# Performance work log

Measured on AMD Instinct MI355X. Metric: run time of the kernel, lower is better.

The kernel has to match this reference:

```python
import jax, jax.numpy as jnp
import numpy as np

N_NODES = 20000
N_EDGES = 160000
N_GRAPHS = 100
IN_CH = 64
EDGE_DIM = 8
NEG_SLOPE = 0.2


def _gatv2(x, edge_index, edge_attr, Wl, Wr, We, att, b, heads, ch, n_nodes):
    # GATv2Conv: e_ij = att . leaky_relu(Wl x_j + Wr x_i [+ We e_ij]), softmax over dst i,
    # out_i = sum_j alpha_ij * (Wl x_j), concat heads, + bias.
    src, dst = edge_index[0], edge_index[1]
    xl = (x @ Wl).reshape(-1, heads, ch)  # [N,H,C] source-side transform
    xr = (x @ Wr).reshape(-1, heads, ch)  # [N,H,C] target-side transform
    m = xl[src] + xr[dst]                 # [E,H,C]
    if edge_attr is not None:
        m = m + (edge_attr @ We).reshape(-1, heads, ch)
    m = jax.nn.leaky_relu(m, NEG_SLOPE)
    logit = jnp.einsum('ehc,hc->eh', m, att)                     # [E,H]
    mx = jax.ops.segment_max(logit, dst, num_segments=n_nodes)   # [N,H]
    ex = jnp.exp(logit - mx[dst])
    den = jax.ops.segment_sum(ex, dst, num_segments=n_nodes)     # [N,H]
    alpha = ex / (den[dst] + 1e-16)                              # [E,H]
    out = jax.ops.segment_sum(alpha[:, :, None] * xl[src], dst, num_segments=n_nodes)
    return out.reshape(-1, heads * ch) + b


def setup_inputs() -> dict:
    key = jax.random.key(0)
    ks = jax.random.split(key, 24)
    def rn(k, shape, fan_in):
        return jax.random.normal(k, shape, dtype=jnp.float32) / np.sqrt(fan_in)
    inp = {}
    inp['x'] = jax.random.normal(ks[0], (N_NODES, IN_CH), dtype=jnp.float32)
    inp['edge_attr'] = jax.random.uniform(ks[1], (N_EDGES, EDGE_DIM), dtype=jnp.float32)
    inp['Wl1'] = rn(ks[2], (IN_CH, 1024), IN_CH)
    inp['Wr1'] = rn(ks[3], (IN_CH, 1024), IN_CH)
    inp['We1'] = rn(ks[4], (EDGE_DIM, 1024), EDGE_DIM)
    inp['att1'] = rn(ks[5], (4, 256), 256)
    inp['b1'] = jnp.zeros((1024,), jnp.float32)
    inp['Wl2'] = rn(ks[6], (1024, 256), 1024)
    inp['Wr2'] = rn(ks[7], (1024, 256), 1024)
    inp['We2'] = rn(ks[8], (EDGE_DIM, 256), EDGE_DIM)
    inp['att2'] = rn(ks[9], (4, 64), 64)
    inp['b2'] = jnp.zeros((256,), jnp.float32)
    inp['Wlp'] = rn(ks[10], (256, 384), 256)
    inp['Wrp'] = rn(ks[11], (256, 384), 256)
    inp['attp'] = rn(ks[12], (6, 64), 64)
    inp['bp'] = jnp.zeros((384,), jnp.float32)
    inp['Wfc1'] = rn(ks[13], (384, 64), 384)
    inp['bfc1'] = jnp.zeros((64,), jnp.float32)
    inp['Wfc2'] = rn(ks[14], (64, 1), 64)
    inp['bfc2'] = jnp.zeros((1,), jnp.float32)
    inp['edge_index'] = jax.random.randint(ks[15], (2, N_EDGES), 0, N_NODES, dtype=jnp.int32)
    inp['edge_index_master'] = jax.random.randint(ks[16], (2, N_EDGES), 0, N_NODES, dtype=jnp.int32)
    inp['n_nodes'] = jnp.full((N_GRAPHS,), N_NODES // N_GRAPHS, dtype=jnp.int32)
    return inp


def reference(x, edge_attr, Wl1, Wr1, We1, att1, b1, Wl2, Wr2, We2, att2, b2,
              Wlp, Wrp, attp, bp, Wfc1, bfc1, Wfc2, bfc2,
              edge_index, edge_index_master, n_nodes):
    h = _gatv2(x, edge_index, edge_attr, Wl1, Wr1, We1, att1, b1, 4, 256, N_NODES)
    h = jax.nn.relu(h)
    h = _gatv2(h, edge_index, edge_attr, Wl2, Wr2, We2, att2, b2, 4, 64, N_NODES)
    h = jax.nn.relu(h)
    h = _gatv2(h, edge_index_master, None, Wlp, Wrp, None, attp, bp, 6, 64, N_NODES)
    last_idx = jnp.cumsum(n_nodes) - 1          # master node = last node of each graph
    master = h[last_idx]                        # [G,384] (dropout p=0 -> identity)
    z = jax.nn.relu(master @ Wfc1 + bfc1)
    return z @ Wfc2 + bfc2                      # [G,1]
```

## Files before the change

### kernel.cpp

```cpp
#include <hip/hip_runtime.h>
#include <hip/hip_bf16.h>

#define DIV_UP(a,b) (((a)+(b)-1)/(b))

typedef __attribute__((ext_vector_type(8))) short short8;
typedef __attribute__((ext_vector_type(4))) float floatx4;
typedef _Float16 half2t __attribute__((ext_vector_type(2)));

static __device__ __forceinline__ unsigned short f2bf(float v) {
    unsigned u = __builtin_bit_cast(unsigned, v);
    u += 0x7fffu + ((u >> 16) & 1u);
    return (unsigned short)(u >> 16);
}
static __device__ __forceinline__ float bflo(unsigned v) {
    return __builtin_bit_cast(float, v << 16);
}
static __device__ __forceinline__ float bfhi(unsigned v) {
    return __builtin_bit_cast(float, v & 0xffff0000u);
}
static __device__ __forceinline__ float fexp2(float x) { return __builtin_amdgcn_exp2f(x); }

static __device__ __forceinline__ unsigned packh2(float lo, float hi) {
    half2t h; h[0] = (_Float16)lo; h[1] = (_Float16)hi;
    return __builtin_bit_cast(unsigned, h);
}
static __device__ __forceinline__ float fdot2(unsigned a, unsigned b, float c) {
    return __builtin_amdgcn_fdot2(__builtin_bit_cast(half2t, a),
                                  __builtin_bit_cast(half2t, b), c, false);
}
static __device__ __forceinline__ unsigned uget(const uint4 v, int k) {
    return k == 0 ? v.x : k == 1 ? v.y : k == 2 ? v.z : v.w;
}

template <int CPL> struct RawT;
template <> struct RawT<8> { using T = uint4; };
template <> struct RawT<4> { using T = uint2; };
template <> struct RawT<2> { using T = unsigned; };

template <int CPL>
static __device__ __forceinline__ void unpackx(const typename RawT<CPL>::T& v, float* d) {
    if constexpr (CPL == 8) {
        d[0] = bflo(v.x); d[1] = bfhi(v.x);
        d[2] = bflo(v.y); d[3] = bfhi(v.y);
        d[4] = bflo(v.z); d[5] = bfhi(v.z);
        d[6] = bflo(v.w); d[7] = bfhi(v.w);
    } else if constexpr (CPL == 4) {
        d[0] = bflo(v.x); d[1] = bfhi(v.x);
        d[2] = bflo(v.y); d[3] = bfhi(v.y);
    } else {
        d[0] = bflo(v); d[1] = bfhi(v);
    }
}

template <int CPL>
static __device__ __forceinline__ void store_bf16v(unsigned short* p, const float* s) {
    unsigned short tmp[CPL];
#pragma unroll
    for (int c = 0; c < CPL; ++c) tmp[c] = f2bf(s[c]);
    if constexpr (CPL == 8) *(uint4*)p = *(uint4*)tmp;
    else if constexpr (CPL == 4) *(ushort4*)p = *(ushort4*)tmp;
    else if constexpr (CPL == 2) *(ushort2*)p = *(ushort2*)tmp;
    else p[0] = tmp[0];
}

template <int CTRL>
static __device__ __forceinline__ float dpp_mv(float x) {
    int r = __builtin_amdgcn_update_dpp(0, __builtin_bit_cast(int, x), CTRL, 0xF, 0xF, false);
    return __builtin_bit_cast(float, r);
}
template <int G>
static __device__ __forceinline__ float group_reduce(float x) {
    x += dpp_mv<0xB1>(x);
    x += dpp_mv<0x4E>(x);
    x += dpp_mv<0x124>(x);
    x += dpp_mv<0x128>(x);
    if constexpr (G >= 32) x += __shfl_xor(x, 16, 64);
    if constexpr (G >= 64) x += __shfl_xor(x, 32, 64);
    return x;
}

static __device__ __forceinline__ void tr_pair(const float* Wa, const float* Wb, int K, int Nn,
                                               unsigned short* Wt, int i) {
    int tot = K * Nn;
    const float* W = (i < tot) ? Wa : Wb;
    unsigned short* dst = Wt + ((i < tot) ? 0 : (size_t)Nn * K);
    int ii = (i < tot) ? i : i - tot;
    int k = ii % K, n = ii / K;
    dst[(size_t)n * K + k] = f2bf(W[(size_t)k * Nn + n]);
}

__global__ void prep_all(const float* __restrict__ x,
                         const float* __restrict__ Wl1, const float* __restrict__ Wr1,
                         const float* __restrict__ Wl2, const float* __restrict__ Wr2,
                         const float* __restrict__ Wlp, const float* __restrict__ Wrp,
                         unsigned short* __restrict__ xbf,
                         unsigned short* __restrict__ wt1, unsigned short* __restrict__ wt2,
                         unsigned short* __restrict__ wt3, int N) {
    const int S1 = 2 * 64 * 1024, S2 = 2 * 1024 * 256, S3 = 2 * 256 * 384;
    int id = blockIdx.x * blockDim.x + threadIdx.x;
    if (id < S1) tr_pair(Wl1, Wr1, 64, 1024, wt1, id);
    else if (id < S1 + S2) tr_pair(Wl2, Wr2, 1024, 256, wt2, id - S1);
    else if (id < S1 + S2 + S3) tr_pair(Wlp, Wrp, 256, 384, wt3, id - S1 - S2);
    else {
        int i = id - S1 - S2 - S3;
        if (i < N * 64) xbf[i] = f2bf(x[i]);
    }
}

#define GLOAD_LDS16(gp, lp) \
    __builtin_amdgcn_global_load_lds((const __attribute__((address_space(1))) void*)(gp), \
                                     (__attribute__((address_space(3))) void*)(lp), 16, 0, 0)

__global__ __launch_bounds__(256) void gemm_mfma(
    const unsigned short* __restrict__ A, const unsigned short* __restrict__ Bt,
    unsigned short* __restrict__ CL, unsigned short* __restrict__ CR,
    int M, int NL, int K) {
    __shared__ unsigned short As[128 * 32];
    __shared__ unsigned short Bs[128 * 32];
    const int tid = threadIdx.x;
    const int m0 = blockIdx.y * 128, n0 = blockIdx.x * 128;
    const bool left = (n0 < NL);
    unsigned short* Cb = left ? CL : CR;
    const int nbase = left ? n0 : n0 - NL;
    const int wave = tid >> 6, lane = tid & 63;
    const int wm = (wave >> 1) * 64, wn = (wave & 1) * 64;
    const int r15 = lane & 15, quad = lane >> 4;
    const int srow = lane >> 2, scol = (lane & 3) * 8;
    const int arow0 = m0 + 32 * wave + srow;
    const int brow0 = n0 + 32 * wave + srow;
    const unsigned short* ap0 = A + (size_t)arow0 * K + scol;
    const unsigned short* ap1 = ap0 + (size_t)16 * K;
    const unsigned short* bp0 = Bt + (size_t)brow0 * K + scol;
    const unsigned short* bp1 = bp0 + (size_t)16 * K;
    unsigned short* alds0 = As + (32 * wave) * 32;
    unsigned short* alds1 = alds0 + 16 * 32;
    unsigned short* blds0 = Bs + (32 * wave) * 32;
    unsigned short* blds1 = blds0 + 16 * 32;
    const bool av0 = arow0 < M, av1 = (arow0 + 16) < M;
    floatx4 acc[4][4];
#pragma unroll
    for (int i = 0; i < 4; ++i)
#pragma unroll
        for (int j = 0; j < 4; ++j) acc[i][j] = (floatx4)0.f;

    for (int k0 = 0; k0 < K; k0 += 32) {
        if (av0) GLOAD_LDS16(ap0, alds0);
        if (av1) GLOAD_LDS16(ap1, alds1);
        GLOAD_LDS16(bp0, blds0);
        GLOAD_LDS16(bp1, blds1);
        ap0 += 32; ap1 += 32; bp0 += 32; bp1 += 32;
        __syncthreads();
        short8 af[4], bfr[4];
#pragma unroll
        for (int i = 0; i < 4; ++i)
            af[i] = *(const short8*)(&As[(wm + i * 16 + r15) * 32 + quad * 8]);
#pragma unroll
        for (int j = 0; j < 4; ++j)
            bfr[j] = *(const short8*)(&Bs[(wn + j * 16 + r15) * 32 + quad * 8]);
#pragma unroll
        for (int i = 0; i < 4; ++i)
#pragma unroll
            for (int j = 0; j < 4; ++j)
                acc[i][j] = __builtin_amdgcn_mfma_f32_16x16x32_bf16(af[i], bfr[j], acc[i][j], 0, 0, 0);
        __syncthreads();
    }
#pragma unroll
    for (int i = 0; i < 4; ++i)
#pragma unroll
        for (int j = 0; j < 4; ++j)
#pragma unroll
            for (int r = 0; r < 4; ++r) {
                int m = m0 + wm + i * 16 + quad * 4 + r;
                int n = nbase + wn + j * 16 + r15;
                if (m < M) Cb[(size_t)m * NL + n] = f2bf(acc[i][j][r]);
            }
}

__global__ void count2_kernel(const int* __restrict__ dst0, const int* __restrict__ dst1,
                              int E, int N, int* __restrict__ cnt) {
    int e = blockIdx.x * blockDim.x + threadIdx.x;
    if (e < E) atomicAdd(&cnt[dst0[e]], 1);
    else if (e < 2 * E) atomicAdd(&cnt[N + dst1[e - E]], 1);
}

__global__ __launch_bounds__(1024) void scan_kernel(const int* __restrict__ cnt_all, int N,
                                                    int* __restrict__ off_all, int* __restrict__ cur_all) {
    const int* cnt = cnt_all + blockIdx.x * N;
    int* off = off_all + blockIdx.x * (N + 1);
    int* cur = cur_all + blockIdx.x * N;
    __shared__ int part[1024];
    int t = threadIdx.x;
    int per = (N + 1023) >> 10;
    int base = t * per;
    int s = 0;
    for (int i = 0; i < per; ++i) { int idx = base + i; if (idx < N) s += cnt[idx]; }
    part[t] = s;
    __syncthreads();
    for (int d2 = 1; d2 < 1024; d2 <<= 1) {
        int v = (t >= d2) ? part[t - d2] : 0;
        __syncthreads();
        part[t] += v;
        __syncthreads();
    }
    int pre = (t == 0) ? 0 : part[t - 1];
    for (int i = 0; i < per; ++i) {
        int idx = base + i;
        if (idx < N) { off[idx] = pre; cur[idx] = pre; pre += cnt[idx]; }
    }
    if (t == 1023) off[N] = part[1023];
}

__global__ void fill2_kernel(const int* __restrict__ src0, const int* __restrict__ dst0,
                             const int* __restrict__ src1, const int* __restrict__ dst1,
                             int E, int N, int* __restrict__ cur, int2* __restrict__ edges,
                             int* __restrict__ srcs) {
    int e = blockIdx.x * blockDim.x + threadIdx.x;
    if (e < E) {
        int p = atomicAdd(&cur[dst0[e]], 1);
        edges[p] = make_int2(src0[e], e);
        srcs[p] = src0[e];
    } else if (e < 2 * E) {
        int i = e - E;
        int p = atomicAdd(&cur[N + dst1[i]], 1);
        srcs[E + p] = src1[i];
    }
}

__global__ void ea_gather_kernel(const float* __restrict__ ea, const int2* __restrict__ edges,
                                 uint4* __restrict__ ead, int E) {
    int j = blockIdx.x * blockDim.x + threadIdx.x;
    if (j >= E) return;
    int ey = edges[j].y;
    const float4* s = (const float4*)(ea + (size_t)ey * 8);
    float4 a = s[0], b = s[1];
    uint4 o;
    o.x = packh2(a.x, a.y);
    o.y = packh2(a.z, a.w);
    o.z = packh2(b.x, b.y);
    o.w = packh2(b.z, b.w);
    ead[j] = o;
}

template <int D, int CPL, int G, int NE>
static __device__ __forceinline__ void hase_group(
    const unsigned short* __restrict__ xl, const uint4* __restrict__ ej,
    const int* __restrict__ sj, const unsigned* wbu,
    const float (&att_r)[CPL], const float (&xr_r)[CPL], int c0,
    float& m, float& l, float (&acc)[CPL]) {
    int src[NE];
#pragma unroll
    for (int n = 0; n < NE; ++n) src[n] = sj[n];
    uint4 ev[NE];
#pragma unroll
    for (int n = 0; n < NE; ++n) ev[n] = ej[n];
    float xv[NE][CPL], z[NE][CPL];
#pragma unroll
    for (int n = 0; n < NE; ++n) {
        typename RawT<CPL>::T xw =
            *(const typename RawT<CPL>::T*)(xl + (size_t)src[n] * D + c0);
        unpackx<CPL>(xw, xv[n]);
#pragma unroll
        for (int c = 0; c < CPL; ++c) z[n][c] = xv[n][c] + xr_r[c];
    }
#pragma unroll
    for (int kp = 0; kp < 4; ++kp) {
#pragma unroll
        for (int q = 0; q < CPL / 4; ++q) {
            uint4 w4 = *(const uint4*)(wbu + kp * D + q * 256);
#pragma unroll
            for (int n = 0; n < NE; ++n) {
                unsigned ep = uget(ev[n], kp);
                z[n][q * 4 + 0] = fdot2(ep, w4.x, z[n][q * 4 + 0]);
                z[n][q * 4 + 1] = fdot2(ep, w4.y, z[n][q * 4 + 1]);
                z[n][q * 4 + 2] = fdot2(ep, w4.z, z[n][q * 4 + 2]);
                z[n][q * 4 + 3] = fdot2(ep, w4.w, z[n][q * 4 + 3]);
            }
        }
    }
    float lg[NE];
#pragma unroll
    for (int n = 0; n < NE; ++n) {
        float t = 0.f;
#pragma unroll
        for (int c = 0; c < CPL; ++c) {
            float a = z[n][c] > 0.f ? z[n][c] : 0.2f * z[n][c];
            t = fmaf(att_r[c], a, t);
        }
        lg[n] = group_reduce<G>(t);
    }
    float mn = m;
#pragma unroll
    for (int n = 0; n < NE; ++n) mn = fmaxf(mn, lg[n]);
    float sc = fexp2(m - mn);
    float p[NE], ps = 0.f;
#pragma unroll
    for (int n = 0; n < NE; ++n) { p[n] = fexp2(lg[n] - mn); ps += p[n]; }
    m = mn;
    l = fmaf(l, sc, ps);
#pragma unroll
    for (int c = 0; c < CPL; ++c) {
        float t = p[0] * xv[0][c];
#pragma unroll
        for (int n = 1; n < NE; ++n) t = fmaf(p[n], xv[n][c], t);
        acc[c] = fmaf(acc[c], sc, t);
    }
}

template <int D, int C, int CB, int WPN, bool RELU>
__global__ __launch_bounds__(256) void attn_hase(
    const unsigned short* __restrict__ xl, const unsigned short* __restrict__ xr,
    const uint4* __restrict__ ead4,
    const float* __restrict__ We, const float* __restrict__ att,
    const int* __restrict__ srcs, const int* __restrict__ off,
    const float* __restrict__ bias, unsigned short* __restrict__ outp, int N) {
    constexpr int CPL = CB / 64;
    constexpr int HW = CB / C;
    constexpr int G = 64 / HW;
    constexpr int NPB = 4 / WPN;
    __shared__ unsigned wsh[4 * D];
    for (int idx = threadIdx.x; idx < D; idx += 256) {
        int kp = idx / (D / 4);
        int t = idx - kp * (D / 4);
        int pos = 4 * t;
        int b = pos / CB;
        int r = pos - b * CB;
        int q = r >> 8;
        int ln4 = r - (q << 8);
        int cc = b * CB + (ln4 >> 2) * CPL + q * 4;
        float4 w0 = *(const float4*)(We + (size_t)(2 * kp) * D + cc);
        float4 w1 = *(const float4*)(We + (size_t)(2 * kp + 1) * D + cc);
        uint4 o;
        o.x = packh2(w0.x, w1.x);
        o.y = packh2(w0.y, w1.y);
        o.z = packh2(w0.z, w1.z);
        o.w = packh2(w0.w, w1.w);
        ((uint4*)wsh)[idx] = o;
    }
    __syncthreads();

    const int wid = threadIdx.x >> 6, lane = threadIdx.x & 63;
    const int wv = wid % WPN, wn = wid / WPN;
    const int c0 = wv * CB + lane * CPL;
    const unsigned* wbu = wsh + wv * CB + lane * 4;

    const float L2E = 1.4426950408889634f;
    float att_r[CPL];
#pragma unroll
    for (int c = 0; c < CPL; ++c) att_r[c] = att[c0 + c] * L2E;

    for (int node = blockIdx.x * NPB + wn; node < N; node += gridDim.x * NPB) {
        typename RawT<CPL>::T xrw =
            *(const typename RawT<CPL>::T*)(xr + (size_t)node * D + c0);
        float xr_r[CPL];
        unpackx<CPL>(xrw, xr_r);
        float m = -1e30f, l = 0.f, acc[CPL];
#pragma unroll
        for (int c = 0; c < CPL; ++c) acc[c] = 0.f;

        const int jb = __builtin_amdgcn_readfirstlane(off[node]);
        const int je = __builtin_amdgcn_readfirstlane(off[node + 1]);
        int j = jb;
        for (; j + 4 <= je; j += 4)
            hase_group<D, CPL, G, 4>(xl, ead4 + j, srcs + j, wbu, att_r, xr_r, c0, m, l, acc);
        for (; j < je; ++j)
            hase_group<D, CPL, G, 1>(xl, ead4 + j, srcs + j, wbu, att_r, xr_r, c0, m, l, acc);

        float inv = 1.f / (l + 1e-16f);
        float r[CPL];
#pragma unroll
        for (int c = 0; c < CPL; ++c) {
            r[c] = fmaf(acc[c], inv, bias[c0 + c]);
            if constexpr (RELU) r[c] = fmaxf(r[c], 0.f);
        }
        store_bf16v<CPL>(outp + (size_t)node * D + c0, r);
    }
}

template <int D, int CPL, int G, int NE>
static __device__ __forceinline__ void noe_group(
    const unsigned short* __restrict__ xl, const int* __restrict__ sj,
    const float (&att_r)[CPL], const float (&xr_r)[CPL], int c0,
    float& m, float& l, float (&acc)[CPL]) {
    int src[NE];
#pragma unroll
    for (int n = 0; n < NE; ++n) src[n] = sj[n];
    float xv[NE][CPL], lg[NE];
#pragma unroll
    for (int n = 0; n < NE; ++n) {
        typename RawT<CPL>::T xw =
            *(const typename RawT<CPL>::T*)(xl + (size_t)src[n] * D + c0);
        unpackx<CPL>(xw, xv[n]);
    }
#pragma unroll
    for (int n = 0; n < NE; ++n) {
        float t = 0.f;
#pragma unroll
        for (int c = 0; c < CPL; ++c) {
            float z = xv[n][c] + xr_r[c];
            z = z > 0.f ? z : 0.2f * z;
            t = fmaf(att_r[c], z, t);
        }
        lg[n] = group_reduce<G>(t);
    }
    float mn = m;
#pragma unroll
    for (int n = 0; n < NE; ++n) mn = fmaxf(mn, lg[n]);
    float sc = fexp2(m - mn);
    float p[NE], ps = 0.f;
#pragma unroll
    for (int n = 0; n < NE; ++n) { p[n] = fexp2(lg[n] - mn); ps += p[n]; }
    m = mn;
    l = fmaf(l, sc, ps);
#pragma unroll
    for (int c = 0; c < CPL; ++c) {
        float t = p[0] * xv[0][c];
#pragma unroll
        for (int n = 1; n < NE; ++n) t = fmaf(p[n], xv[n][c], t);
        acc[c] = fmaf(acc[c], sc, t);
    }
}

template <int D, int C, int CB, bool RELU>
static __device__ __forceinline__ void attn_wave3(
    const unsigned short* __restrict__ xl, const unsigned short* __restrict__ xr,
    const float* __restrict__ att,
    const int* __restrict__ srcs, int jb, int je,
    const float* __restrict__ bias, float* __restrict__ outp,
    int node, int cb, int lane) {
    constexpr int CPL = CB / 64;
    constexpr int HW = CB / C;
    constexpr int G = 64 / HW;
    const int c0 = cb + lane * CPL;
    const float L2E = 1.4426950408889634f;

    typename RawT<CPL>::T xrw =
        *(const typename RawT<CPL>::T*)(xr + (size_t)node * D + c0);
    float xr_r[CPL], att_r[CPL];
    unpackx<CPL>(xrw, xr_r);
#pragma unroll
    for (int c = 0; c < CPL; ++c) att_r[c] = att[c0 + c] * L2E;

    float m = -1e30f, l = 0.f, acc[CPL];
#pragma unroll
    for (int c = 0; c < CPL; ++c) acc[c] = 0.f;

    int j = jb;
    for (; j + 4 <= je; j += 4)
        noe_group<D, CPL, G, 4>(xl, srcs + j, att_r, xr_r, c0, m, l, acc);
    for (; j < je; ++j)
        noe_group<D, CPL, G, 1>(xl, srcs + j, att_r, xr_r, c0, m, l, acc);

    float inv = 1.f / (l + 1e-16f);
    float* out = outp + (size_t)node * D + c0;
    float tmp[CPL];
#pragma unroll
    for (int c = 0; c < CPL; ++c) {
        float r = fmaf(acc[c], inv, bias[c0 + c]);
        if constexpr (RELU) r = fmaxf(r, 0.f);
        tmp[c] = r;
    }
    if constexpr (CPL == 4) *(float4*)out = *(float4*)tmp;
    else if constexpr (CPL == 2) *(float2*)out = *(float2*)tmp;
    else out[0] = tmp[0];
}

template <int D, int C, int CB0, int CB1, bool RELU>
__global__ __launch_bounds__(256) void attn_noe(
    const unsigned short* __restrict__ xl, const unsigned short* __restrict__ xr,
    const float* __restrict__ att,
    const int* __restrict__ srcs, const int* __restrict__ off,
    const float* __restrict__ bias, float* __restrict__ outp, int N) {
    const int wid = threadIdx.x >> 6, lane = threadIdx.x & 63;
    const int gw = blockIdx.x * 4 + wid;
    const int node = gw >> 1, wv = gw & 1;
    if (node >= N) return;
    const int jb = __builtin_amdgcn_readfirstlane(off[node]);
    const int je = __builtin_amdgcn_readfirstlane(off[node + 1]);
    if (wv == 0)
        attn_wave3<D, C, CB0, RELU>(xl, xr, att, srcs, jb, je, bias, outp, node, 0, lane);
    else
        attn_wave3<D, C, CB1, RELU>(xl, xr, att, srcs, jb, je, bias, outp, node, CB0, lane);
}

__global__ void mlp_kernel(const float* __restrict__ h3, const int* __restrict__ nn,
                           const float* __restrict__ Wfc1, const float* __restrict__ bfc1,
                           const float* __restrict__ Wfc2, const float* __restrict__ bfc2,
                           float* __restrict__ out, int G) {
    int g = blockIdx.x, t = threadIdx.x;
    int s = 0;
    for (int k = 0; k <= g; ++k) s += nn[k];
    const float* row = h3 + (size_t)(s - 1) * 384;
    float z = bfc1[t];
    for (int k = 0; k < 384; ++k) z = fmaf(row[k], Wfc1[k * 64 + t], z);
    z = fmaxf(z, 0.f);
    float v = z * Wfc2[t];
#pragma unroll
    for (int o = 32; o; o >>= 1) v += __shfl_xor(v, o, 64);
    if (t == 0) out[g] = v + bfc2[0];
}

extern "C" void kernel_launch(void* const* d_in, const int* in_sizes, int n_in,
                              void* d_out, int out_size, void* d_ws, size_t ws_size,
                              hipStream_t stream) {
    const float* x    = (const float*)d_in[0];
    const float* ea   = (const float*)d_in[1];
    const float* Wl1  = (const float*)d_in[2];
    const float* Wr1  = (const float*)d_in[3];
    const float* We1  = (const float*)d_in[4];
    const float* att1 = (const float*)d_in[5];
    const float* b1   = (const float*)d_in[6];
    const float* Wl2  = (const float*)d_in[7];
    const float* Wr2  = (const float*)d_in[8];
    const float* We2  = (const float*)d_in[9];
    const float* att2 = (const float*)d_in[10];
    const float* b2   = (const float*)d_in[11];
    const float* Wlp  = (const float*)d_in[12];
    const float* Wrp  = (const float*)d_in[13];
    const float* attp = (const float*)d_in[14];
    const float* bp   = (const float*)d_in[15];
    const float* Wfc1 = (const float*)d_in[16];
    const float* bfc1 = (const float*)d_in[17];
    const float* Wfc2 = (const float*)d_in[18];
    const float* bfc2 = (const float*)d_in[19];
    const int* ei     = (const int*)d_in[20];
    const int* eim    = (const int*)d_in[21];
    const int* nn     = (const int*)d_in[22];

    const int N = in_sizes[0] / 64;
    const int E = in_sizes[20] / 2;
    const int G = in_sizes[22];
    const int* src1 = ei,  *dst1 = ei + E;
    const int* srcm = eim, *dstm = eim + E;

    char* w = (char*)d_ws;
    size_t o = 0;
    auto alloc = [&](size_t b) { size_t r = o; o += (b + 255) & ~(size_t)255; return r; };
    char* R1 = w + alloc((size_t)N * 2048 * 2);
    unsigned short* xl1 = (unsigned short*)R1;
    unsigned short* xr1 = xl1 + (size_t)N * 1024;
    unsigned short* xl3 = (unsigned short*)R1;
    unsigned short* xr3 = xl3 + (size_t)N * 384;
    float* h3 = (float*)(R1 + (size_t)N * 768 * 2 + 256);
    unsigned short* h1   = (unsigned short*)(w + alloc((size_t)N * 1024 * 2));
    char* R2 = w + alloc((size_t)N * 512 * 2);
    unsigned short* xl2 = (unsigned short*)R2;
    unsigned short* xr2 = xl2 + (size_t)N * 256;
    unsigned short* h2   = (unsigned short*)(w + alloc((size_t)N * 256 * 2));
    unsigned short* xbf  = (unsigned short*)(w + alloc((size_t)N * 64 * 2));
    unsigned short* wt1  = (unsigned short*)(w + alloc((size_t)2048 * 64 * 2));
    unsigned short* wt2  = (unsigned short*)(w + alloc((size_t)512 * 1024 * 2));
    unsigned short* wt3  = (unsigned short*)(w + alloc((size_t)768 * 256 * 2));
    int*  cnt   = (int*)(w + alloc((size_t)2 * N * 4));
    int*  off   = (int*)(w + alloc((size_t)2 * (N + 1) * 4));
    int*  cur   = (int*)(w + alloc((size_t)2 * N * 4));
    char* eReg  = w + alloc((size_t)2 * E * 8 + 4096);
    int2* edges = (int2*)eReg;
    int*  srcs  = (int*)(eReg + (size_t)E * 8);
    (void)ws_size; (void)n_in; (void)out_size;

    uint4* ead1 = (uint4*)R2;
    uint4* ead2 = (uint4*)h1;

    dim3 blk(256);

    {
        int tot = 2 * 64 * 1024 + 2 * 1024 * 256 + 2 * 256 * 384 + N * 64;
        prep_all<<<DIV_UP(tot, 256), blk, 0, stream>>>(x, Wl1, Wr1, Wl2, Wr2, Wlp, Wrp,
                                                       xbf, wt1, wt2, wt3, N);
    }

    hipMemsetAsync(cnt, 0, (size_t)2 * N * 4, stream);
    count2_kernel<<<DIV_UP(2 * E, 256), blk, 0, stream>>>(dst1, dstm, E, N, cnt);
    scan_kernel<<<2, 1024, 0, stream>>>(cnt, N, off, cur);
    fill2_kernel<<<DIV_UP(2 * E, 256), blk, 0, stream>>>(src1, dst1, srcm, dstm, E, N, cur,
                                                         edges, srcs);
    ea_gather_kernel<<<DIV_UP(E, 256), blk, 0, stream>>>(ea, edges, ead1, E);
    const int* off3 = off + (N + 1);
    const int* srcs3 = srcs + E;

    gemm_mfma<<<dim3(2048 / 128, DIV_UP(N, 128)), blk, 0, stream>>>(
        xbf, wt1, xl1, xr1, N, 1024, 64);
    attn_hase<1024, 256, 512, 2, true><<<2560, blk, 0, stream>>>(
        xl1, xr1, ead1, We1, att1, srcs, off, b1, h1, N);

    gemm_mfma<<<dim3(512 / 128, DIV_UP(N, 128)), blk, 0, stream>>>(
        h1, wt2, xl2, xr2, N, 256, 1024);
    ea_gather_kernel<<<DIV_UP(E, 256), blk, 0, stream>>>(ea, edges, ead2, E);
    attn_hase<256, 64, 256, 1, true><<<1280, blk, 0, stream>>>(
        xl2, xr2, ead2, We2, att2, srcs, off, b2, h2, N);

    gemm_mfma<<<dim3(768 / 128, DIV_UP(N, 128)), blk, 0, stream>>>(
        h2, wt3, xl3, xr3, N, 384, 256);
    attn_noe<384, 64, 256, 128, false><<<DIV_UP(N, 2), blk, 0, stream>>>(
        xl3, xr3, attp, srcs3, off3, bp, h3, N);

    mlp_kernel<<<G, 64, 0, stream>>>(h3, nn, Wfc1, bfc1, Wfc2, bfc2, (float*)d_out, G);
}
```

Before: 416.0 us.

## Switch intermediate features to fp16 and compute attention logits with packed half2 math

The GEMM epilogue now writes xl/xr as fp16 instead of bf16. The edge attention kernels then build logits with packed half2 adds, FMAs and max-based leaky ReLU, plus fdot2 against att. Edge attributes are stored as duplicated half2 pairs (two uint4 per edge) and the edge weights are re-laid out per k row, so the edge projection becomes packed FMAs. This roughly halves the VALU work per channel in the logit path. In exchange it doubles edge-attribute storage and bandwidth, and fp16 accumulation of the logit terms risks precision loss or overflow compared with the fp32 path.

```diff
diff --git a/kernel.cpp b/kernel.cpp
--- a/kernel.cpp
+++ b/kernel.cpp
@@ -12,25 +12,26 @@
     u += 0x7fffu + ((u >> 16) & 1u);
     return (unsigned short)(u >> 16);
 }
-static __device__ __forceinline__ float bflo(unsigned v) {
-    return __builtin_bit_cast(float, v << 16);
-}
-static __device__ __forceinline__ float bfhi(unsigned v) {
-    return __builtin_bit_cast(float, v & 0xffff0000u);
+static __device__ __forceinline__ unsigned short f2h(float v) {
+    _Float16 h = (_Float16)v;
+    return __builtin_bit_cast(unsigned short, h);
 }
 static __device__ __forceinline__ float fexp2(float x) { return __builtin_amdgcn_exp2f(x); }
 
-static __device__ __forceinline__ unsigned packh2(float lo, float hi) {
-    half2t h; h[0] = (_Float16)lo; h[1] = (_Float16)hi;
-    return __builtin_bit_cast(unsigned, h);
-}
-static __device__ __forceinline__ float fdot2(unsigned a, unsigned b, float c) {
-    return __builtin_amdgcn_fdot2(__builtin_bit_cast(half2t, a),
-                                  __builtin_bit_cast(half2t, b), c, false);
+static __device__ __forceinline__ half2t mk_h2(float lo, float hi) {
+    half2t h; h[0] = (_Float16)lo; h[1] = (_Float16)hi; return h;
+}
+static __device__ __forceinline__ unsigned ph2(float lo, float hi) {
+    return __builtin_bit_cast(unsigned, mk_h2(lo, hi));
+}
+static __device__ __forceinline__ float fdot2h(half2t a, half2t b, float c) {
+    return __builtin_amdgcn_fdot2(a, b, c, false);
 }
 static __device__ __forceinline__ unsigned uget(const uint4 v, int k) {
     return k == 0 ? v.x : k == 1 ? v.y : k == 2 ? v.z : v.w;
 }
+static __device__ __forceinline__ float h2lo(half2t h) { return (float)h[0]; }
+static __device__ __forceinline__ float h2hi(half2t h) { return (float)h[1]; }
 
 template <int CPL> struct RawT;
 template <> struct RawT<8> { using T = uint4; };
@@ -38,17 +39,20 @@
 template <> struct RawT<2> { using T = unsigned; };
 
 template <int CPL>
-static __device__ __forceinline__ void unpackx(const typename RawT<CPL>::T& v, float* d) {
+static __device__ __forceinline__ void loadh2(const unsigned short* p, half2t* d) {
     if constexpr (CPL == 8) {
-        d[0] = bflo(v.x); d[1] = bfhi(v.x);
-        d[2] = bflo(v.y); d[3] = bfhi(v.y);
-        d[4] = bflo(v.z); d[5] = bfhi(v.z);
-        d[6] = bflo(v.w); d[7] = bfhi(v.w);
+        uint4 v = *(const uint4*)p;
+        d[0] = __builtin_bit_cast(half2t, v.x);
+        d[1] = __builtin_bit_cast(half2t, v.y);
+        d[2] = __builtin_bit_cast(half2t, v.z);
+        d[3] = __builtin_bit_cast(half2t, v.w);
     } else if constexpr (CPL == 4) {
-        d[0] = bflo(v.x); d[1] = bfhi(v.x);
-        d[2] = bflo(v.y); d[3] = bfhi(v.y);
+        uint2 v = *(const uint2*)p;
+        d[0] = __builtin_bit_cast(half2t, v.x);
+        d[1] = __builtin_bit_cast(half2t, v.y);
     } else {
-        d[0] = bflo(v); d[1] = bfhi(v);
+        unsigned v = *(const unsigned*)p;
+        d[0] = __builtin_bit_cast(half2t, v);
     }
 }
 
@@ -172,7 +176,7 @@
             for (int r = 0; r < 4; ++r) {
                 int m = m0 + wm + i * 16 + quad * 4 + r;
                 int n = nbase + wn + j * 16 + r15;
-                if (m < M) Cb[(size_t)m * NL + n] = f2bf(acc[i][j][r]);
+                if (m < M) Cb[(size_t)m * NL + n] = f2h(acc[i][j][r]);
             }
 }
 
@@ -233,58 +237,68 @@
     int ey = edges[j].y;
     const float4* s = (const float4*)(ea + (size_t)ey * 8);
     float4 a = s[0], b = s[1];
-    uint4 o;
-    o.x = packh2(a.x, a.y);
-    o.y = packh2(a.z, a.w);
-    o.z = packh2(b.x, b.y);
-    o.w = packh2(b.z, b.w);
-    ead[j] = o;
+    uint4 o0, o1;
+    o0.x = ph2(a.x, a.x); o0.y = ph2(a.y, a.y);
+    o0.z = ph2(a.z, a.z); o0.w = ph2(a.w, a.w);
+    o1.x = ph2(b.x, b.x); o1.y = ph2(b.y, b.y);
+    o1.z = ph2(b.z, b.z); o1.w = ph2(b.w, b.w);
+    ead[2 * j]     = o0;
+    ead[2 * j + 1] = o1;
 }
 
 template <int D, int CPL, int G, int NE>
 static __device__ __forceinline__ void hase_group(
     const unsigned short* __restrict__ xl, const uint4* __restrict__ ej,
     const int* __restrict__ sj, const unsigned* wbu,
-    const float (&att_r)[CPL], const float (&xr_r)[CPL], int c0,
+    const half2t (&att2)[CPL / 2], const half2t (&xr2)[CPL / 2], int c0,
     float& m, float& l, float (&acc)[CPL]) {
+    constexpr int P = CPL / 2;
     int src[NE];
 #pragma unroll
     for (int n = 0; n < NE; ++n) src[n] = sj[n];
-    uint4 ev[NE];
-#pragma unroll
-    for (int n = 0; n < NE; ++n) ev[n] = ej[n];
-    float xv[NE][CPL], z[NE][CPL];
+    uint4 ev0[NE], ev1[NE];
+#pragma unroll
+    for (int n = 0; n < NE; ++n) { ev0[n] = ej[2 * n]; ev1[n] = ej[2 * n + 1]; }
+    half2t xv[NE][P], z[NE][P];
 #pragma unroll
     for (int n = 0; n < NE; ++n) {
-        typename RawT<CPL>::T xw =
-            *(const typename RawT<CPL>::T*)(xl + (size_t)src[n] * D + c0);
-        unpackx<CPL>(xw, xv[n]);
-#pragma unroll
-        for (int c = 0; c < CPL; ++c) z[n][c] = xv[n][c] + xr_r[c];
-    }
-#pragma unroll
-    for (int kp = 0; kp < 4; ++kp) {
-#pragma unroll
-        for (int q = 0; q < CPL / 4; ++q) {
-            uint4 w4 = *(const uint4*)(wbu + kp * D + q * 256);
-#pragma unroll
-            for (int n = 0; n < NE; ++n) {
-                unsigned ep = uget(ev[n], kp);
-                z[n][q * 4 + 0] = fdot2(ep, w4.x, z[n][q * 4 + 0]);
-                z[n][q * 4 + 1] = fdot2(ep, w4.y, z[n][q * 4 + 1]);
-                z[n][q * 4 + 2] = fdot2(ep, w4.z, z[n][q * 4 + 2]);
-                z[n][q * 4 + 3] = fdot2(ep, w4.w, z[n][q * 4 + 3]);
-            }
+        loadh2<CPL>(xl + (size_t)src[n] * D + c0, xv[n]);
+#pragma unroll
+        for (int p = 0; p < P; ++p) z[n][p] = xv[n][p] + xr2[p];
+    }
+#pragma unroll
+    for (int k = 0; k < 8; ++k) {
+        half2t wk[P];
+        if constexpr (CPL == 8) {
+            uint4 w4 = *(const uint4*)(wbu + k * (D / 2));
+            wk[0] = __builtin_bit_cast(half2t, w4.x);
+            wk[1] = __builtin_bit_cast(half2t, w4.y);
+            wk[2] = __builtin_bit_cast(half2t, w4.z);
+            wk[3] = __builtin_bit_cast(half2t, w4.w);
+        } else {
+            uint2 w2 = *(const uint2*)(wbu + k * (D / 2));
+            wk[0] = __builtin_bit_cast(half2t, w2.x);
+            wk[1] = __builtin_bit_cast(half2t, w2.y);
         }
-    }
+#pragma unroll
+        for (int n = 0; n < NE; ++n) {
+            unsigned eu = (k < 4) ? uget(ev0[n], k) : uget(ev1[n], k - 4);
+            half2t e2 = __builtin_bit_cast(half2t, eu);
+#pragma unroll
+            for (int p = 0; p < P; ++p)
+                z[n][p] = __builtin_elementwise_fma(e2, wk[p], z[n][p]);
+        }
+    }
+    const half2t c02 = mk_h2(0.2f, 0.2f);
     float lg[NE];
 #pragma unroll
     for (int n = 0; n < NE; ++n) {
         float t = 0.f;
 #pragma unroll
-        for (int c = 0; c < CPL; ++c) {
-            float a = z[n][c] > 0.f ? z[n][c] : 0.2f * z[n][c];
-            t = fmaf(att_r[c], a, t);
+        for (int p = 0; p < P; ++p) {
+            half2t zz = z[n][p];
+            half2t lz = __builtin_elementwise_max(zz, zz * c02);
+            t = fdot2h(att2[p], lz, t);
         }
         lg[n] = group_reduce<G>(t);
     }
@@ -292,17 +306,22 @@
 #pragma unroll
     for (int n = 0; n < NE; ++n) mn = fmaxf(mn, lg[n]);
     float sc = fexp2(m - mn);
-    float p[NE], ps = 0.f;
-#pragma unroll
-    for (int n = 0; n < NE; ++n) { p[n] = fexp2(lg[n] - mn); ps += p[n]; }
+    float pr[NE], ps = 0.f;
+#pragma unroll
+    for (int n = 0; n < NE; ++n) { pr[n] = fexp2(lg[n] - mn); ps += pr[n]; }
     m = mn;
     l = fmaf(l, sc, ps);
 #pragma unroll
-    for (int c = 0; c < CPL; ++c) {
-        float t = p[0] * xv[0][c];
-#pragma unroll
-        for (int n = 1; n < NE; ++n) t = fmaf(p[n], xv[n][c], t);
-        acc[c] = fmaf(acc[c], sc, t);
+    for (int p = 0; p < P; ++p) {
+        float t0 = pr[0] * h2lo(xv[0][p]);
+        float t1 = pr[0] * h2hi(xv[0][p]);
+#pragma unroll
+        for (int n = 1; n < NE; ++n) {
+            t0 = fmaf(pr[n], h2lo(xv[n][p]), t0);
+            t1 = fmaf(pr[n], h2hi(xv[n][p]), t1);
+        }
+        acc[2 * p]     = fmaf(acc[2 * p],     sc, t0);
+        acc[2 * p + 1] = fmaf(acc[2 * p + 1], sc, t1);
     }
 }
 
@@ -314,45 +333,33 @@
     const int* __restrict__ srcs, const int* __restrict__ off,
     const float* __restrict__ bias, unsigned short* __restrict__ outp, int N) {
     constexpr int CPL = CB / 64;
+    constexpr int P = CPL / 2;
     constexpr int HW = CB / C;
     constexpr int G = 64 / HW;
     constexpr int NPB = 4 / WPN;
     __shared__ unsigned wsh[4 * D];
-    for (int idx = threadIdx.x; idx < D; idx += 256) {
-        int kp = idx / (D / 4);
-        int t = idx - kp * (D / 4);
-        int pos = 4 * t;
-        int b = pos / CB;
-        int r = pos - b * CB;
-        int q = r >> 8;
-        int ln4 = r - (q << 8);
-        int cc = b * CB + (ln4 >> 2) * CPL + q * 4;
-        float4 w0 = *(const float4*)(We + (size_t)(2 * kp) * D + cc);
-        float4 w1 = *(const float4*)(We + (size_t)(2 * kp + 1) * D + cc);
-        uint4 o;
-        o.x = packh2(w0.x, w1.x);
-        o.y = packh2(w0.y, w1.y);
-        o.z = packh2(w0.z, w1.z);
-        o.w = packh2(w0.w, w1.w);
-        ((uint4*)wsh)[idx] = o;
+    for (int idx = threadIdx.x; idx < 4 * D; idx += 256) {
+        int k = idx / (D / 2);
+        int r = idx - k * (D / 2);
+        int c = 2 * r;
+        wsh[idx] = ph2(We[(size_t)k * D + c], We[(size_t)k * D + c + 1]);
     }
     __syncthreads();
 
     const int wid = threadIdx.x >> 6, lane = threadIdx.x & 63;
     const int wv = wid % WPN, wn = wid / WPN;
     const int c0 = wv * CB + lane * CPL;
-    const unsigned* wbu = wsh + wv * CB + lane * 4;
+    const unsigned* wbu = wsh + wv * (CB / 2) + lane * (CPL / 2);
 
     const float L2E = 1.4426950408889634f;
-    float att_r[CPL];
-#pragma unroll
-    for (int c = 0; c < CPL; ++c) att_r[c] = att[c0 + c] * L2E;
+    half2t att2[P];
+#pragma unroll
+    for (int p = 0; p < P; ++p)
+        att2[p] = mk_h2(att[c0 + 2 * p] * L2E, att[c0 + 2 * p + 1] * L2E);
 
     for (int node = blockIdx.x * NPB + wn; node < N; node += gridDim.x * NPB) {
-        typename RawT<CPL>::T xrw =
-            *(const typename RawT<CPL>::T*)(xr + (size_t)node * D + c0);
-        float xr_r[CPL];
-        unpackx<CPL>(xrw, xr_r);
+        half2t xr2[P];
+        loadh2<CPL>(xr + (size_t)node * D + c0, xr2);
         float m = -1e30f, l = 0.f, acc[CPL];
 #pragma unroll
         for (int c = 0; c < CPL; ++c) acc[c] = 0.f;
@@ -361,9 +368,9 @@
         const int je = __builtin_amdgcn_readfirstlane(off[node + 1]);
         int j = jb;
         for (; j + 4 <= je; j += 4)
-            hase_group<D, CPL, G, 4>(xl, ead4 + j, srcs + j, wbu, att_r, xr_r, c0, m, l, acc);
+            hase_group<D, CPL, G, 4>(xl, ead4 + 2 * j, srcs + j, wbu, att2, xr2, c0, m, l, acc);
         for (; j < je; ++j)
-            hase_group<D, CPL, G, 1>(xl, ead4 + j, srcs + j, wbu, att_r, xr_r, c0, m, l, acc);
+            hase_group<D, CPL, G, 1>(xl, ead4 + 2 * j, srcs + j, wbu, att2, xr2, c0, m, l, acc);
 
         float inv = 1.f / (l + 1e-16f);
         float r[CPL];
@@ -379,26 +386,26 @@
 template <int D, int CPL, int G, int NE>
 static __device__ __forceinline__ void noe_group(
     const unsigned short* __restrict__ xl, const int* __restrict__ sj,
-    const float (&att_r)[CPL], const float (&xr_r)[CPL], int c0,
+    const half2t (&att2)[CPL / 2], const half2t (&xr2)[CPL / 2], int c0,
     float& m, float& l, float (&acc)[CPL]) {
+    constexpr int P = CPL / 2;
     int src[NE];
 #pragma unroll
     for (int n = 0; n < NE; ++n) src[n] = sj[n];
-    float xv[NE][CPL], lg[NE];
-#pragma unroll
-    for (int n = 0; n < NE; ++n) {
-        typename RawT<CPL>::T xw =
-            *(const typename RawT<CPL>::T*)(xl + (size_t)src[n] * D + c0);
-        unpackx<CPL>(xw, xv[n]);
-    }
+    half2t xv[NE][P];
+#pragma unroll
+    for (int n = 0; n < NE; ++n)
+        loadh2<CPL>(xl + (size_t)src[n] * D + c0, xv[n]);
+    const half2t c02 = mk_h2(0.2f, 0.2f);
+    float lg[NE];
 #pragma unroll
     for (int n = 0; n < NE; ++n) {
         float t = 0.f;
 #pragma unroll
-        for (int c = 0; c < CPL; ++c) {
-            float z = xv[n][c] + xr_r[c];
-            z = z > 0.f ? z : 0.2f * z;
-            t = fmaf(att_r[c], z, t);
+        for (int p = 0; p < P; ++p) {
+            half2t zz = xv[n][p] + xr2[p];
+            half2t lz = __builtin_elementwise_max(zz, zz * c02);
+            t = fdot2h(att2[p], lz, t);
         }
         lg[n] = group_reduce<G>(t);
     }
@@ -406,17 +413,22 @@
 #pragma unroll
     for (int n = 0; n < NE; ++n) mn = fmaxf(mn, lg[n]);
     float sc = fexp2(m - mn);
-    float p[NE], ps = 0.f;
-#pragma unroll
-    for (int n = 0; n < NE; ++n) { p[n] = fexp2(lg[n] - mn); ps += p[n]; }
+    float pr[NE], ps = 0.f;
+#pragma unroll
+    for (int n = 0; n < NE; ++n) { pr[n] = fexp2(lg[n] - mn); ps += pr[n]; }
     m = mn;
     l = fmaf(l, sc, ps);
 #pragma unroll
-    for (int c = 0; c < CPL; ++c) {
-        float t = p[0] * xv[0][c];
-#pragma unroll
-        for (int n = 1; n < NE; ++n) t = fmaf(p[n], xv[n][c], t);
-        acc[c] = fmaf(acc[c], sc, t);
+    for (int p = 0; p < P; ++p) {
+        float t0 = pr[0] * h2lo(xv[0][p]);
+        float t1 = pr[0] * h2hi(xv[0][p]);
+#pragma unroll
+        for (int n = 1; n < NE; ++n) {
+            t0 = fmaf(pr[n], h2lo(xv[n][p]), t0);
+            t1 = fmaf(pr[n], h2hi(xv[n][p]), t1);
+        }
+        acc[2 * p]     = fmaf(acc[2 * p],     sc, t0);
+        acc[2 * p + 1] = fmaf(acc[2 * p + 1], sc, t1);
     }
 }
 
@@ -428,17 +440,17 @@
     const float* __restrict__ bias, float* __restrict__ outp,
     int node, int cb, int lane) {
     constexpr int CPL = CB / 64;
+    constexpr int P = CPL / 2;
     constexpr int HW = CB / C;
     constexpr int G = 64 / HW;
     const int c0 = cb + lane * CPL;
     const float L2E = 1.4426950408889634f;
 
-    typename RawT<CPL>::T xrw =
-        *(const typename RawT<CPL>::T*)(xr + (size_t)node * D + c0);
-    float xr_r[CPL], att_r[CPL];
-    unpackx<CPL>(xrw, xr_r);
-#pragma unroll
-    for (int c = 0; c < CPL; ++c) att_r[c] = att[c0 + c] * L2E;
+    half2t xr2[P], att2[P];
+    loadh2<CPL>(xr + (size_t)node * D + c0, xr2);
+#pragma unroll
+    for (int p = 0; p < P; ++p)
+        att2[p] = mk_h2(att[c0 + 2 * p] * L2E, att[c0 + 2 * p + 1] * L2E);
 
     float m = -1e30f, l = 0.f, acc[CPL];
 #pragma unroll
@@ -446,9 +458,9 @@
 
     int j = jb;
     for (; j + 4 <= je; j += 4)
-        noe_group<D, CPL, G, 4>(xl, srcs + j, att_r, xr_r, c0, m, l, acc);
+        noe_group<D, CPL, G, 4>(xl, srcs + j, att2, xr2, c0, m, l, acc);
     for (; j < je; ++j)
-        noe_group<D, CPL, G, 1>(xl, srcs + j, att_r, xr_r, c0, m, l, acc);
+        noe_group<D, CPL, G, 1>(xl, srcs + j, att2, xr2, c0, m, l, acc);
 
     float inv = 1.f / (l + 1e-16f);
     float* out = outp + (size_t)node * D + c0;
```

After: 420.5 us. No clear change (+1.1%).
